# Optimization experiments

Measured on AMD Instinct MI355X. Metric: run time of the kernel, lower is better.

## Reference

```python
import jax, jax.numpy as jnp
import numpy as np

B, D_IN, H, D_OUT = 8192, 1024, 4096, 1024


def setup_inputs() -> dict:
    key = jax.random.key(0)
    ks = jax.random.split(key, 8)
    return {
        "X": jax.random.normal(ks[0], (B, D_IN), jnp.float32),
        "state": jax.random.normal(ks[1], (B, H), jnp.float32),
        "W_in": jax.random.normal(ks[2], (H, D_IN), jnp.float32) * (2.0 / D_IN) ** 0.5,
        "b_in": jax.random.normal(ks[3], (H,), jnp.float32) * 0.1,
        "W_rec": jax.random.normal(ks[4], (H, H), jnp.float32) * (2.0 / H) ** 0.5,
        "b_rec": jax.random.normal(ks[5], (H,), jnp.float32) * 0.1,
        "W_out": jax.random.normal(ks[6], (D_OUT, H), jnp.float32) * (2.0 / H) ** 0.5,
        "b_out": jax.random.normal(ks[7], (D_OUT,), jnp.float32) * 0.1,
    }


def reference(X, state, W_in, b_in, W_rec, b_rec, W_out, b_out):
    # Single vanilla RNN cell step (ReLU recurrence), matching VanillaRNN.forward.
    # state: [B, H] = ReLU(X @ W_in^T + b_in + state @ W_rec^T + b_rec)
    new_state = jax.nn.relu(X @ W_in.T + b_in + state @ W_rec.T + b_rec)
    # out: [B, D_OUT] = ReLU(new_state @ W_out^T + b_out)
    out = jax.nn.relu(new_state @ W_out.T + b_out)
    return out, new_state
```

## Files before the change

kernel.cpp:

```cpp
#include <hip/hip_runtime.h>
#include <hip/hip_bf16.h>
#include <stdint.h>
#include <stddef.h>

#define BSZ  8192
#define DIN  1024
#define HH   4096
#define DOUT 1024

#define BM 128
#define BN 128
#define BK 32

typedef __attribute__((ext_vector_type(8))) short   frag8;
typedef __attribute__((ext_vector_type(4))) float   f32x4;
typedef __attribute__((ext_vector_type(8))) unsigned short u16x8;

__device__ __forceinline__ unsigned short f2bf_rne(float f) {
    union { float f; uint32_t u; } c; c.f = f;
    uint32_t u = c.u;
    return (unsigned short)((u + 0x7FFFu + ((u >> 16) & 1u)) >> 16);
}

__device__ __forceinline__ void cvt8(const float* __restrict__ s, unsigned short* __restrict__ d) {
    f32x4 v0 = *(const f32x4*)s;
    f32x4 v1 = *(const f32x4*)(s + 4);
    u16x8 o;
    o[0] = f2bf_rne(v0[0]); o[1] = f2bf_rne(v0[1]); o[2] = f2bf_rne(v0[2]); o[3] = f2bf_rne(v0[3]);
    o[4] = f2bf_rne(v1[0]); o[5] = f2bf_rne(v1[1]); o[6] = f2bf_rne(v1[2]); o[7] = f2bf_rne(v1[3]);
    *(u16x8*)d = o;
}

__global__ __launch_bounds__(256)
void cvt_f32_bf16(const float* __restrict__ src, unsigned short* __restrict__ dst, long n) {
    long i = ((long)blockIdx.x * 256 + threadIdx.x) * 8;
    if (i < n) cvt8(src + i, dst + i);
}

__global__ __launch_bounds__(256)
void cvt_all5(const float* __restrict__ s0, unsigned short* __restrict__ d0, long n0,
              const float* __restrict__ s1, unsigned short* __restrict__ d1, long n1,
              const float* __restrict__ s2, unsigned short* __restrict__ d2, long n2,
              const float* __restrict__ s3, unsigned short* __restrict__ d3, long n3,
              const float* __restrict__ s4, unsigned short* __restrict__ d4, long n4) {
    long i = ((long)blockIdx.x * 256 + threadIdx.x) * 8;
    if (i < n0) { cvt8(s0 + i, d0 + i); return; } i -= n0;
    if (i < n1) { cvt8(s1 + i, d1 + i); return; } i -= n1;
    if (i < n2) { cvt8(s2 + i, d2 + i); return; } i -= n2;
    if (i < n3) { cvt8(s3 + i, d3 + i); return; } i -= n3;
    if (i < n4) { cvt8(s4 + i, d4 + i); }
}

__device__ __forceinline__ void glds16(const unsigned short* __restrict__ gp, short* lp) {
    __builtin_amdgcn_global_load_lds(
        (const __attribute__((address_space(1))) uint32_t*)gp,
        (__attribute__((address_space(3))) uint32_t*)lp, 16, 0, 0);
}

template <bool A_BF16, bool B_BF16>
__global__ __launch_bounds__(256)
void gemm_bt_relu(const void* __restrict__ A1, int lda1,
                  const void* __restrict__ A2, int lda2,
                  const void* __restrict__ B1, int ldb1,
                  const void* __restrict__ B2, int ldb2,
                  int Ksplit, int K,
                  const float* __restrict__ bias1, const float* __restrict__ bias2,
                  float* __restrict__ C, unsigned short* __restrict__ Cb, int N) {
    __shared__ short As[BM * BK];
    __shared__ short Bs[BN * BK];

    const int tid    = threadIdx.x;
    const int tile_m = blockIdx.y * BM;
    const int tile_n = blockIdx.x * BN;
    const int wave = tid >> 6, lane = tid & 63;
    const int quad = lane >> 4, l16 = lane & 15;
    const int wm = (wave >> 1) * 64;
    const int wn = (wave & 1) * 64;
    const int sr = tid >> 2;
    const int sc = (tid & 3) * 8;

    short* ldsA0 = &As[tid * 8]; short* ldsA1 = &As[(256 + tid) * 8];
    short* ldsB0 = &Bs[tid * 8]; short* ldsB1 = &Bs[(256 + tid) * 8];

    f32x4 acc[4][4] = {};

    for (int phase = 0; phase < 2; ++phase) {
        const int kmax = phase ? (K - Ksplit) : Ksplit;
        if (kmax <= 0) continue;
        const void* Ap = phase ? A2 : A1; const int la = phase ? lda2 : lda1;
        const void* Bp = phase ? B2 : B1; const int lb = phase ? ldb2 : ldb1;

        const unsigned short *ga = nullptr, *gb = nullptr;
        const float *fa = nullptr, *fb = nullptr;
        if (A_BF16) ga = (const unsigned short*)Ap + (size_t)(tile_m + sr) * la + sc;
        else        fa = (const float*)Ap          + (size_t)(tile_m + sr) * la + sc;
        if (B_BF16) gb = (const unsigned short*)Bp + (size_t)(tile_n + sr) * lb + sc;
        else        fb = (const float*)Bp          + (size_t)(tile_n + sr) * lb + sc;
        const size_t la64 = (size_t)64 * la, lb64 = (size_t)64 * lb;

        for (int kk = 0; kk < kmax; kk += BK) {
            __syncthreads();
            if (A_BF16) {
                glds16(ga, ldsA0); glds16(ga + la64, ldsA1); ga += BK;
            } else {
                unsigned short t0[8], t1[8];
                cvt8(fa, t0); cvt8(fa + la64, t1); fa += BK;
                *(u16x8*)ldsA0 = *(u16x8*)t0; *(u16x8*)ldsA1 = *(u16x8*)t1;
            }
            if (B_BF16) {
                glds16(gb, ldsB0); glds16(gb + lb64, ldsB1); gb += BK;
            } else {
                unsigned short t0[8], t1[8];
                cvt8(fb, t0); cvt8(fb + lb64, t1); fb += BK;
                *(u16x8*)ldsB0 = *(u16x8*)t0; *(u16x8*)ldsB1 = *(u16x8*)t1;
            }
            __syncthreads();

            frag8 af[4], bfr[4];
#pragma unroll
            for (int i = 0; i < 4; i++)
                af[i] = *(const frag8*)&As[(wm + i * 16 + l16) * BK + quad * 8];
#pragma unroll
            for (int i = 0; i < 4; i++)
                bfr[i] = *(const frag8*)&Bs[(wn + i * 16 + l16) * BK + quad * 8];
#pragma unroll
            for (int mi = 0; mi < 4; mi++)
#pragma unroll
                for (int ni = 0; ni < 4; ni++)
                    acc[mi][ni] = __builtin_amdgcn_mfma_f32_16x16x32_bf16(
                        af[mi], bfr[ni], acc[mi][ni], 0, 0, 0);
        }
    }

#pragma unroll
    for (int mi = 0; mi < 4; mi++) {
        const int m0 = tile_m + wm + mi * 16 + quad * 4;
#pragma unroll
        for (int ni = 0; ni < 4; ni++) {
            const int n = tile_n + wn + ni * 16 + l16;
            float bv = bias1[n];
            if (bias2) bv += bias2[n];
#pragma unroll
            for (int r = 0; r < 4; r++) {
                float v = acc[mi][ni][r] + bv;
                v = v > 0.f ? v : 0.f;
                const size_t idx = (size_t)(m0 + r) * N + n;
                C[idx] = v;
                if (Cb) Cb[idx] = f2bf_rne(v);
            }
        }
    }
}

extern "C" void kernel_launch(void* const* d_in, const int* in_sizes, int n_in,
                              void* d_out, int out_size, void* d_ws, size_t ws_size,
                              hipStream_t stream) {
    const float* X     = (const float*)d_in[0];
    const float* state = (const float*)d_in[1];
    const float* W_in  = (const float*)d_in[2];
    const float* b_in  = (const float*)d_in[3];
    const float* W_rec = (const float*)d_in[4];
    const float* b_rec = (const float*)d_in[5];
    const float* W_out = (const float*)d_in[6];
    const float* b_out = (const float*)d_in[7];

    float* out       = (float*)d_out;
    float* new_state = out + (size_t)BSZ * DOUT;

    const size_t nX = (size_t)BSZ * DIN, nS = (size_t)BSZ * HH;
    const size_t nWin = (size_t)HH * DIN, nWrec = (size_t)HH * HH, nWout = (size_t)DOUT * HH;

    const size_t offX = 0;
    const size_t offS = offX + nX * 2;
    const size_t offWin = offS + nS * 2;
    const size_t offWrec = offWin + nWin * 2;
    const size_t offWout = offWrec + nWrec * 2;
    const size_t offNS = offWout + nWout * 2;
    const size_t need_full = offNS + nS * 2;
    const size_t need_mid = nS * 2 + nWout * 2;

    char* ws = (char*)d_ws;
    const dim3 blk(256);
    const dim3 g1(HH / BN, BSZ / BM);
    const dim3 g2(DOUT / BN, BSZ / BM);

    if (ws_size >= need_full) {
        unsigned short* Xb    = (unsigned short*)(ws + offX);
        unsigned short* Sb    = (unsigned short*)(ws + offS);
        unsigned short* Winb  = (unsigned short*)(ws + offWin);
        unsigned short* Wrecb = (unsigned short*)(ws + offWrec);
        unsigned short* Woutb = (unsigned short*)(ws + offWout);
        unsigned short* NSb   = (unsigned short*)(ws + offNS);
        const long total = (long)(nX + nS + nWin + nWrec + nWout);
        cvt_all5<<<dim3((unsigned)((total / 8 + 255) / 256)), blk, 0, stream>>>(
            X, Xb, (long)nX, state, Sb, (long)nS, W_in, Winb, (long)nWin,
            W_rec, Wrecb, (long)nWrec, W_out, Woutb, (long)nWout);
        gemm_bt_relu<true, true><<<g1, blk, 0, stream>>>(
            Xb, DIN, Sb, HH, Winb, DIN, Wrecb, HH, DIN, DIN + HH,
            b_in, b_rec, new_state, NSb, HH);
        gemm_bt_relu<true, true><<<g2, blk, 0, stream>>>(
            NSb, HH, NSb, HH, Woutb, HH, Woutb, HH, HH, HH,
            b_out, nullptr, out, nullptr, DOUT);
    } else if (ws_size >= need_mid) {
        unsigned short* NSb   = (unsigned short*)ws;
        unsigned short* Woutb = (unsigned short*)(ws + nS * 2);
        cvt_f32_bf16<<<dim3((unsigned)((nWout / 8 + 255) / 256)), blk, 0, stream>>>(
            W_out, Woutb, (long)nWout);
        gemm_bt_relu<false, false><<<g1, blk, 0, stream>>>(
            X, DIN, state, HH, W_in, DIN, W_rec, HH, DIN, DIN + HH,
            b_in, b_rec, new_state, NSb, HH);
        gemm_bt_relu<true, true><<<g2, blk, 0, stream>>>(
            NSb, HH, NSb, HH, Woutb, HH, Woutb, HH, HH, HH,
            b_out, nullptr, out, nullptr, DOUT);
    } else {
        gemm_bt_relu<false, false><<<g1, blk, 0, stream>>>(
            X, DIN, state, HH, W_in, DIN, W_rec, HH, DIN, DIN + HH,
            b_in, b_rec, new_state, nullptr, HH);
        gemm_bt_relu<false, false><<<g2, blk, 0, stream>>>(
            new_state, HH, new_state, HH, W_out, HH, W_out, HH, HH, HH,
            b_out, nullptr, out, nullptr, DOUT);
    }
}
```

Baseline: 903.2 us.

## Replace 128x128 GEMM with pipelined 256x256 swizzled-LDS kernel and packed operands

The conversion kernel now packs X and state into one concatenated bf16 matrix, and W_in and W_rec into another, so the first GEMM runs over a single K=5120 operand pair. A new 512-thread GEMM kernel uses 256x256 tiles with K=64 steps, double-buffered XOR-swizzled LDS filled by direct global-to-LDS loads, and prefetch interleaved across phases with raised wave priority around the MFMA blocks. Larger tiles are meant to raise arithmetic intensity and hide load latency. In exchange the kernel uses 128KB of dynamic LDS and much more register pressure, and only the full-workspace path uses it.

After: 750.7 us. -16.9%, faster.

```diff
diff --git a/kernel.cpp b/kernel.cpp
--- a/kernel.cpp
+++ b/kernel.cpp
@@ -51,10 +51,179 @@
     if (i < n4) { cvt8(s4 + i, d4 + i); }
 }
 
+#define NX8  ((long)BSZ * DIN / 8)
+#define NS8  ((long)BSZ * HH / 8)
+#define NWI8 ((long)HH * DIN / 8)
+#define NWR8 ((long)HH * HH / 8)
+#define NWO8 ((long)DOUT * HH / 8)
+#define NCVT_BLOCKS 32768
+
+__global__ __launch_bounds__(256)
+void cvt_pack(const float* __restrict__ X, const float* __restrict__ S,
+              const float* __restrict__ Wi, const float* __restrict__ Wr,
+              const float* __restrict__ Wo,
+              unsigned short* __restrict__ XS, unsigned short* __restrict__ W1,
+              unsigned short* __restrict__ Wob) {
+    long i = (long)blockIdx.x * 256 + threadIdx.x;
+    if (i < NX8)  { long r = i >> 7, c = i & 127; cvt8(X + i * 8, XS + r * 5120 + c * 8); return; }
+    i -= NX8;
+    if (i < NS8)  { long r = i >> 9, c = i & 511; cvt8(S + i * 8, XS + r * 5120 + 1024 + c * 8); return; }
+    i -= NS8;
+    if (i < NWI8) { long r = i >> 7, c = i & 127; cvt8(Wi + i * 8, W1 + r * 5120 + c * 8); return; }
+    i -= NWI8;
+    if (i < NWR8) { long r = i >> 9, c = i & 511; cvt8(Wr + i * 8, W1 + r * 5120 + 1024 + c * 8); return; }
+    i -= NWR8;
+    if (i < NWO8) { cvt8(Wo + i * 8, Wob + i * 8); }
+}
+
 __device__ __forceinline__ void glds16(const unsigned short* __restrict__ gp, short* lp) {
     __builtin_amdgcn_global_load_lds(
         (const __attribute__((address_space(1))) uint32_t*)gp,
         (__attribute__((address_space(3))) uint32_t*)lp, 16, 0, 0);
+}
+
+__device__ __forceinline__ void glds16v(const unsigned short* __restrict__ gp, void* lp) {
+    __builtin_amdgcn_global_load_lds(
+        (const __attribute__((address_space(1))) uint32_t*)gp,
+        (__attribute__((address_space(3))) uint32_t*)lp, 16, 0, 0);
+}
+
+template<int C>
+__device__ __forceinline__ void ktile_group(
+    int kA, int kB,
+    const unsigned short* __restrict__ gA, size_t a64,
+    const unsigned short* __restrict__ gB, size_t b64,
+    const char* Ar0, const char* Br0, char* ldsw,
+    int aoff, int boff, f32x4 (&acc)[8][4])
+{
+    const char* Ar = Ar0 + C * 65536;
+    const char* Br = Br0 + C * 65536;
+    char* wA = ldsw + (C ^ 1) * 65536;
+    char* wB = ldsw + C * 65536 + 32768;
+    const unsigned short* gAk = gA + kA * 64;
+    const unsigned short* gBk = gB + kB * 64;
+
+    frag8 bfr[4][2];
+    frag8 af[2][2];
+#pragma unroll
+    for (int p = 0; p < 4; ++p) {
+        if (p == 0) {
+#pragma unroll
+            for (int ni = 0; ni < 4; ni++)
+#pragma unroll
+                for (int ks = 0; ks < 2; ks++)
+                    bfr[ni][ks] = *(const frag8*)(Br + ni * 2048 + (boff ^ (ks << 6)));
+        }
+#pragma unroll
+        for (int m2 = 0; m2 < 2; m2++)
+#pragma unroll
+            for (int ks = 0; ks < 2; ks++)
+                af[m2][ks] = *(const frag8*)(Ar + (p * 2 + m2) * 2048 + (aoff ^ (ks << 6)));
+
+        if (p == 0) {
+            glds16v(gAk,           wA);
+            glds16v(gAk + a64,     wA + 8192);
+            glds16v(gAk + 2 * a64, wA + 16384);
+            glds16v(gAk + 3 * a64, wA + 16384 + 8192);
+        } else if (p == 1) {
+            glds16v(gBk,           wB);
+            glds16v(gBk + b64,     wB + 8192);
+        } else if (p == 2) {
+            glds16v(gBk + 2 * b64, wB + 16384);
+            glds16v(gBk + 3 * b64, wB + 16384 + 8192);
+        }
+
+        __builtin_amdgcn_s_barrier();
+        __builtin_amdgcn_s_setprio(1);
+#pragma unroll
+        for (int m2 = 0; m2 < 2; m2++)
+#pragma unroll
+            for (int ni = 0; ni < 4; ni++)
+#pragma unroll
+                for (int ks = 0; ks < 2; ks++)
+                    acc[p * 2 + m2][ni] = __builtin_amdgcn_mfma_f32_16x16x32_bf16(
+                        af[m2][ks], bfr[ni][ks], acc[p * 2 + m2][ni], 0, 0, 0);
+        __builtin_amdgcn_s_setprio(0);
+        if (p == 3) asm volatile("s_waitcnt vmcnt(4)" ::: "memory");
+        __builtin_amdgcn_s_barrier();
+    }
+}
+
+__global__ __launch_bounds__(512, 2)
+void gemm256_relu(const unsigned short* __restrict__ A, int lda,
+                  const unsigned short* __restrict__ B, int ldb, int K,
+                  const float* __restrict__ bias1, const float* __restrict__ bias2,
+                  float* __restrict__ C, unsigned short* __restrict__ Cb, int ncols) {
+    extern __shared__ char lds[];
+
+    const int tid  = threadIdx.x;
+    const int wave = tid >> 6, lane = tid & 63;
+    const int quad = lane >> 4, l16 = lane & 15;
+    const int wm2  = wave >> 2, wn4 = wave & 3;
+    const int tile_m = blockIdx.y * 256;
+    const int tile_n = blockIdx.x * 256;
+    const int NT = K >> 6;
+
+    const int r0 = tid >> 3;
+    const int c0 = (tid & 7) ^ (r0 & 7);
+    const unsigned short* gA = A + (size_t)(tile_m + r0) * lda + c0 * 8;
+    const unsigned short* gB = B + (size_t)(tile_n + r0) * ldb + c0 * 8;
+    const size_t a64 = (size_t)64 * lda, b64 = (size_t)64 * ldb;
+
+    const int swz  = (quad ^ (l16 & 7)) << 4;
+    const int aoff = l16 * 128 + swz;
+    const int boff = ((wn4 & 1) * 64 + l16) * 128 + swz;
+    const char* Ar0 = lds + wm2 * 16384;
+    const char* Br0 = lds + 32768 + (wn4 >> 1) * 16384;
+    char* ldsw = lds + wave * 1024;
+
+    glds16v(gA,           ldsw);
+    glds16v(gA + a64,     ldsw + 8192);
+    glds16v(gA + 2 * a64, ldsw + 16384);
+    glds16v(gA + 3 * a64, ldsw + 16384 + 8192);
+    glds16v(gB,           ldsw + 32768);
+    glds16v(gB + b64,     ldsw + 32768 + 8192);
+    glds16v(gB + 2 * b64, ldsw + 32768 + 16384);
+    glds16v(gB + 3 * b64, ldsw + 32768 + 16384 + 8192);
+    {
+        const unsigned short* gB1 = gB + 64;
+        glds16v(gB1,           ldsw + 65536 + 32768);
+        glds16v(gB1 + b64,     ldsw + 65536 + 32768 + 8192);
+        glds16v(gB1 + 2 * b64, ldsw + 65536 + 32768 + 16384);
+        glds16v(gB1 + 3 * b64, ldsw + 65536 + 32768 + 16384 + 8192);
+    }
+    asm volatile("s_waitcnt vmcnt(4)" ::: "memory");
+    __builtin_amdgcn_s_barrier();
+
+    f32x4 acc[8][4] = {};
+
+    for (int kt = 0; kt < NT; kt += 2) {
+        int kA0 = kt + 1;
+        int kB0 = kt + 2; if (kB0 >= NT) kB0 -= NT;
+        ktile_group<0>(kA0, kB0, gA, a64, gB, b64, Ar0, Br0, ldsw, aoff, boff, acc);
+        int kA1 = kt + 2; if (kA1 >= NT) kA1 -= NT;
+        int kB1 = kt + 3; if (kB1 >= NT) kB1 -= NT;
+        ktile_group<1>(kA1, kB1, gA, a64, gB, b64, Ar0, Br0, ldsw, aoff, boff, acc);
+    }
+
+#pragma unroll
+    for (int ni = 0; ni < 4; ni++) {
+        const int n = tile_n + wn4 * 64 + ni * 16 + l16;
+        float bv = bias1[n];
+        if (bias2) bv += bias2[n];
+#pragma unroll
+        for (int mi = 0; mi < 8; mi++) {
+            const int m0 = tile_m + wm2 * 128 + mi * 16 + quad * 4;
+#pragma unroll
+            for (int r = 0; r < 4; r++) {
+                float v = acc[mi][ni][r] + bv;
+                v = v > 0.f ? v : 0.f;
+                const size_t idx = (size_t)(m0 + r) * ncols + n;
+                C[idx] = v;
+                if (Cb) Cb[idx] = f2bf_rne(v);
+            }
+        }
+    }
 }
 
 template <bool A_BF16, bool B_BF16>
@@ -116,10 +285,10 @@
             }
             __syncthreads();
 
-            frag8 af[4], bfr[4];
+            frag8 af2[4], bfr[4];
 #pragma unroll
             for (int i = 0; i < 4; i++)
-                af[i] = *(const frag8*)&As[(wm + i * 16 + l16) * BK + quad * 8];
+                af2[i] = *(const frag8*)&As[(wm + i * 16 + l16) * BK + quad * 8];
 #pragma unroll
             for (int i = 0; i < 4; i++)
                 bfr[i] = *(const frag8*)&Bs[(wn + i * 16 + l16) * BK + quad * 8];
@@ -128,7 +297,7 @@
 #pragma unroll
                 for (int ni = 0; ni < 4; ni++)
                     acc[mi][ni] = __builtin_amdgcn_mfma_f32_16x16x32_bf16(
-                        af[mi], bfr[ni], acc[mi][ni], 0, 0, 0);
+                        af2[mi], bfr[ni], acc[mi][ni], 0, 0, 0);
         }
     }
 
@@ -170,38 +339,38 @@
     const size_t nX = (size_t)BSZ * DIN, nS = (size_t)BSZ * HH;
     const size_t nWin = (size_t)HH * DIN, nWrec = (size_t)HH * HH, nWout = (size_t)DOUT * HH;
 
-    const size_t offX = 0;
-    const size_t offS = offX + nX * 2;
-    const size_t offWin = offS + nS * 2;
-    const size_t offWrec = offWin + nWin * 2;
-    const size_t offWout = offWrec + nWrec * 2;
-    const size_t offNS = offWout + nWout * 2;
+    const size_t offXS = 0;
+    const size_t offW1 = offXS + (size_t)BSZ * (DIN + HH) * 2;
+    const size_t offWo = offW1 + (size_t)HH  * (DIN + HH) * 2;
+    const size_t offNS = offWo + (size_t)DOUT * HH * 2;
     const size_t need_full = offNS + nS * 2;
     const size_t need_mid = nS * 2 + nWout * 2;
 
     char* ws = (char*)d_ws;
     const dim3 blk(256);
-    const dim3 g1(HH / BN, BSZ / BM);
-    const dim3 g2(DOUT / BN, BSZ / BM);
 
     if (ws_size >= need_full) {
-        unsigned short* Xb    = (unsigned short*)(ws + offX);
-        unsigned short* Sb    = (unsigned short*)(ws + offS);
-        unsigned short* Winb  = (unsigned short*)(ws + offWin);
-        unsigned short* Wrecb = (unsigned short*)(ws + offWrec);
-        unsigned short* Woutb = (unsigned short*)(ws + offWout);
-        unsigned short* NSb   = (unsigned short*)(ws + offNS);
-        const long total = (long)(nX + nS + nWin + nWrec + nWout);
-        cvt_all5<<<dim3((unsigned)((total / 8 + 255) / 256)), blk, 0, stream>>>(
-            X, Xb, (long)nX, state, Sb, (long)nS, W_in, Winb, (long)nWin,
-            W_rec, Wrecb, (long)nWrec, W_out, Woutb, (long)nWout);
-        gemm_bt_relu<true, true><<<g1, blk, 0, stream>>>(
-            Xb, DIN, Sb, HH, Winb, DIN, Wrecb, HH, DIN, DIN + HH,
-            b_in, b_rec, new_state, NSb, HH);
-        gemm_bt_relu<true, true><<<g2, blk, 0, stream>>>(
-            NSb, HH, NSb, HH, Woutb, HH, Woutb, HH, HH, HH,
-            b_out, nullptr, out, nullptr, DOUT);
+        unsigned short* XSb = (unsigned short*)(ws + offXS);
+        unsigned short* W1b = (unsigned short*)(ws + offW1);
+        unsigned short* Wob = (unsigned short*)(ws + offWo);
+        unsigned short* NSb = (unsigned short*)(ws + offNS);
+
+        static bool s_attr = false;
+        if (!s_attr) {
+            hipFuncSetAttribute(reinterpret_cast<const void*>(gemm256_relu),
+                                hipFuncAttributeMaxDynamicSharedMemorySize, 131072);
+            s_attr = true;
+        }
+
+        cvt_pack<<<dim3(NCVT_BLOCKS), blk, 0, stream>>>(
+            X, state, W_in, W_rec, W_out, XSb, W1b, Wob);
+        gemm256_relu<<<dim3(HH / 256, BSZ / 256), dim3(512), 131072, stream>>>(
+            XSb, DIN + HH, W1b, DIN + HH, DIN + HH, b_in, b_rec, new_state, NSb, HH);
+        gemm256_relu<<<dim3(DOUT / 256, BSZ / 256), dim3(512), 131072, stream>>>(
+            NSb, HH, Wob, HH, HH, b_out, nullptr, out, nullptr, DOUT);
     } else if (ws_size >= need_mid) {
+        const dim3 g1(HH / BN, BSZ / BM);
+        const dim3 g2(DOUT / BN, BSZ / BM);
         unsigned short* NSb   = (unsigned short*)ws;
         unsigned short* Woutb = (unsigned short*)(ws + nS * 2);
         cvt_f32_bf16<<<dim3((unsigned)((nWout / 8 + 255) / 256)), blk, 0, stream>>>(
@@ -213,6 +382,8 @@
             NSb, HH, NSb, HH, Woutb, HH, Woutb, HH, HH, HH,
             b_out, nullptr, out, nullptr, DOUT);
     } else {
+        const dim3 g1(HH / BN, BSZ / BM);
+        const dim3 g2(DOUT / BN, BSZ / BM);
         gemm_bt_relu<false, false><<<g1, blk, 0, stream>>>(
             X, DIN, state, HH, W_in, DIN, W_rec, HH, DIN, DIN + HH,
             b_in, b_rec, new_state, nullptr, HH);
```
